# Optimization experiments

Measured on AMD Instinct MI355X. Metric: run time of the kernel, lower is better.

The kernel has to match this reference:

```python
import math
import jax, jax.numpy as jnp
import numpy as np

N_HEADS = 16
TOPK_FACTOR = 0.5

def setup_inputs() -> dict:
    key = jax.random.key(0)
    ks = jax.random.split(key, 11)
    B, L, D = 2, 2048, 1024
    s = 0.02
    return {
        "q": jax.random.normal(ks[0], (B, L, D), jnp.float32),
        "k": jax.random.normal(ks[1], (B, L, D), jnp.float32),
        "v": jax.random.normal(ks[2], (B, L, D), jnp.float32),
        "Wq": jax.random.normal(ks[3], (D, D), jnp.float32) * s,
        "bq": jnp.zeros((D,), jnp.float32),
        "Wk": jax.random.normal(ks[4], (D, D), jnp.float32) * s,
        "bk": jnp.zeros((D,), jnp.float32),
        "Wv": jax.random.normal(ks[5], (D, D), jnp.float32) * s,
        "bv": jnp.zeros((D,), jnp.float32),
        "Wo": jax.random.normal(ks[6], (D, D), jnp.float32) * s,
        "bo": jnp.zeros((D,), jnp.float32),
    }

def reference(q, k, v, Wq, bq, Wk, bk, Wv, bv, Wo, bo):
    B, Lq, D = q.shape
    Lk = k.shape[1]
    H = N_HEADS
    d_k = D // H
    # projections -> [B, H, L, d_k]
    Q = (q @ Wq.T + bq).reshape(B, Lq, H, d_k).transpose(0, 2, 1, 3)
    K = (k @ Wk.T + bk).reshape(B, Lk, H, d_k).transpose(0, 2, 1, 3)
    V = (v @ Wv.T + bv).reshape(B, Lk, H, d_k).transpose(0, 2, 1, 3)
    # dense scores [B, H, Lq, Lk]
    scores = jnp.einsum("bhqd,bhkd->bhqk", Q, K) / math.sqrt(d_k)
    topk = max(1, int(TOPK_FACTOR * Lk))
    topk_scores, topk_idx = jax.lax.top_k(scores, topk)  # [B,H,Lq,topk]
    sm = jax.nn.softmax(topk_scores, axis=-1)
    # scatter softmax probs back into a zero [B,H,Lq,Lk] tensor (dropout in eval = identity)
    b_idx = jnp.arange(B)[:, None, None, None]
    h_idx = jnp.arange(H)[None, :, None, None]
    q_idx = jnp.arange(Lq)[None, None, :, None]
    attn = jnp.zeros_like(scores).at[b_idx, h_idx, q_idx, topk_idx].set(sm)
    ctx = jnp.einsum("bhqk,bhkd->bhqd", attn, V)
    ctx = ctx.transpose(0, 2, 1, 3).reshape(B, Lq, H * d_k)
    return ctx @ Wo.T + bo
```

## Files before the change

kernel.cpp:

```cpp
#include <hip/hip_runtime.h>
#include <math.h>

#define BATCH 2
#define SEQ 2048
#define DM 1024
#define NH 16
#define DH 64
#define TOPKN 1024
#define MROWS (BATCH * SEQ)

typedef float f32x4 __attribute__((ext_vector_type(4)));
typedef short s16x8 __attribute__((ext_vector_type(8)));
typedef short s16x4 __attribute__((ext_vector_type(4)));

#if __has_builtin(__builtin_amdgcn_mfma_f32_16x16x16_bf16)
#define MFMA1616(acc, a, b) acc = __builtin_amdgcn_mfma_f32_16x16x16_bf16(a, b, acc, 0, 0, 0)
#define MFMA1616_FENCE()
#elif __has_builtin(__builtin_amdgcn_mfma_f32_16x16x16bf16_1k)
#define MFMA1616(acc, a, b) acc = __builtin_amdgcn_mfma_f32_16x16x16bf16_1k(a, b, acc, 0, 0, 0)
#define MFMA1616_FENCE()
#else
#define MFMA1616(acc, a, b) \
  asm volatile("v_mfma_f32_16x16x16_bf16 %0, %1, %2, %0" : "+v"(acc) : "v"(a), "v"(b))
#define MFMA1616_FENCE() asm volatile("s_nop 7\ns_nop 7")
#endif

__device__ __forceinline__ unsigned short f2bf(float x) {
  unsigned u = __float_as_uint(x);
  return (unsigned short)((u + 0x7FFFu + ((u >> 16) & 1u)) >> 16);
}
__device__ __forceinline__ unsigned packHL(float x) {
  unsigned h = f2bf(x);
  float r = x - __uint_as_float(h << 16);
  unsigned l = f2bf(r);
  return h | (l << 16);
}

__global__ __launch_bounds__(256) void convW(const float* __restrict__ W,
                                             unsigned short* __restrict__ Whi,
                                             unsigned short* __restrict__ Wlo) {
  int i = (blockIdx.x * 256 + threadIdx.x) * 4;
  float4 x = *(const float4*)&W[i];
  float xs[4] = {x.x, x.y, x.z, x.w};
  union { s16x4 v; unsigned short s[4]; } hu, lu;
#pragma unroll
  for (int e = 0; e < 4; ++e) {
    unsigned short hb = f2bf(xs[e]);
    hu.s[e] = hb;
    lu.s[e] = f2bf(xs[e] - __uint_as_float((unsigned)hb << 16));
  }
  *(s16x4*)&Whi[i] = hu.v;
  *(s16x4*)&Wlo[i] = lu.v;
}

template <int ASRC, int MODE>
__global__ __launch_bounds__(256) void gemm_mfma(
    const void* __restrict__ Asrc, const unsigned short* __restrict__ Whi,
    const unsigned short* __restrict__ Wlo, const float* __restrict__ bias,
    void* __restrict__ out0, void* __restrict__ out1) {
  __shared__ unsigned short Ah[128][64], Al[128][64];
  __shared__ unsigned short Bh[64][64], Bl[64][64];

  const int f = blockIdx.x;
  const int xcd = f & 7, s = f >> 3;
  const int bm = xcd * 4 + (s >> 4);
  const int bn = s & 15;
  const int m0g = bm * 128, n0g = bn * 64;
  const int t = threadIdx.x, w = t >> 6, lane = t & 63;
  const int g = lane >> 4, c = lane & 15;
  const int wm = w >> 1, wn = w & 1;

  f32x4 acc[4][2];
#pragma unroll
  for (int i = 0; i < 4; ++i)
#pragma unroll
    for (int j = 0; j < 2; ++j) acc[i][j] = (f32x4){0.f, 0.f, 0.f, 0.f};

#pragma unroll 1
  for (int k0 = 0; k0 < 1024; k0 += 64) {
#pragma unroll
    for (int i = 0; i < 4; ++i) {
      int oid = t * 4 + i;
      int r = oid >> 3, j = oid & 7;
      union { s16x8 v; unsigned short sh[8]; } hu, lu;
      if (ASRC == 0) {
        const float* src = (const float*)Asrc + (size_t)(m0g + r) * 1024 + k0 + j * 8;
        float4 x0 = *(const float4*)src, x1 = *(const float4*)(src + 4);
        float xs[8] = {x0.x, x0.y, x0.z, x0.w, x1.x, x1.y, x1.z, x1.w};
#pragma unroll
        for (int e = 0; e < 8; ++e) {
          unsigned u = __float_as_uint(xs[e]);
          hu.sh[e] = (unsigned short)(u >> 16);
          lu.sh[e] = f2bf(xs[e] - __uint_as_float(u & 0xFFFF0000u));
        }
      } else {
        const unsigned* src = (const unsigned*)Asrc + (size_t)(m0g + r) * 1024 + k0 + j * 8;
        uint4 u0 = *(const uint4*)src, u1 = *(const uint4*)(src + 4);
        unsigned us[8] = {u0.x, u0.y, u0.z, u0.w, u1.x, u1.y, u1.z, u1.w};
#pragma unroll
        for (int e = 0; e < 8; ++e) {
          hu.sh[e] = (unsigned short)(us[e] & 0xFFFFu);
          lu.sh[e] = (unsigned short)(us[e] >> 16);
        }
      }
      int od = (j ^ (r & 7)) * 8;
      *(s16x8*)&Ah[r][od] = hu.v;
      *(s16x8*)&Al[r][od] = lu.v;
    }
#pragma unroll
    for (int i = 0; i < 4; ++i) {
      int oid = t * 4 + i;
      int pl = oid >> 9, idx = oid & 511, r = idx >> 3, j = idx & 7;
      const unsigned short* src = (pl ? Wlo : Whi) + (size_t)(n0g + r) * 1024 + k0 + j * 8;
      uint4 d = *(const uint4*)src;
      int od = (j ^ (r & 7)) * 8;
      if (pl) *(uint4*)&Bl[r][od] = d; else *(uint4*)&Bh[r][od] = d;
    }
    __syncthreads();
#pragma unroll
    for (int k2 = 0; k2 < 2; ++k2) {
      s16x8 ah[4], al4[4], bh[2], bl[2];
      int ob = ((k2 * 4 + g) ^ (c & 7)) * 8;
#pragma unroll
      for (int i = 0; i < 4; ++i) {
        int r = wm * 64 + i * 16 + c;
        ah[i] = *(const s16x8*)&Ah[r][ob];
        al4[i] = *(const s16x8*)&Al[r][ob];
      }
#pragma unroll
      for (int j = 0; j < 2; ++j) {
        int r = wn * 32 + j * 16 + c;
        bh[j] = *(const s16x8*)&Bh[r][ob];
        bl[j] = *(const s16x8*)&Bl[r][ob];
      }
#pragma unroll
      for (int i = 0; i < 4; ++i)
#pragma unroll
        for (int j = 0; j < 2; ++j) {
          acc[i][j] = __builtin_amdgcn_mfma_f32_16x16x32_bf16(ah[i], bh[j], acc[i][j], 0, 0, 0);
          acc[i][j] = __builtin_amdgcn_mfma_f32_16x16x32_bf16(ah[i], bl[j], acc[i][j], 0, 0, 0);
          acc[i][j] = __builtin_amdgcn_mfma_f32_16x16x32_bf16(al4[i], bh[j], acc[i][j], 0, 0, 0);
        }
    }
    __syncthreads();
  }

#pragma unroll
  for (int j = 0; j < 2; ++j) {
    const int col = n0g + wn * 32 + j * 16 + c;
    const float bj = bias[col];
#pragma unroll
    for (int i = 0; i < 4; ++i) {
      const int row0 = m0g + wm * 64 + i * 16 + g * 4;
      if (MODE == 0) {
        float* O = (float*)out0;
#pragma unroll
        for (int rr = 0; rr < 4; ++rr)
          O[(size_t)(row0 + rr) * 1024 + col] = acc[i][j][rr] + bj;
      } else if (MODE == 1) {
        unsigned* Q = (unsigned*)out0;
#pragma unroll
        for (int rr = 0; rr < 4; ++rr)
          Q[(size_t)(row0 + rr) * 1024 + col] = packHL((acc[i][j][rr] + bj) * 0.125f);
      } else if (MODE == 2) {
        unsigned short* Khi = (unsigned short*)out0;
        unsigned short* Klo = (unsigned short*)out1;
#pragma unroll
        for (int rr = 0; rr < 4; ++rr) {
          float x = acc[i][j][rr] + bj;
          unsigned short hb = f2bf(x);
          Khi[(size_t)(row0 + rr) * 1024 + col] = hb;
          Klo[(size_t)(row0 + rr) * 1024 + col] = f2bf(x - __uint_as_float((unsigned)hb << 16));
        }
      } else {
        unsigned short* Vt = (unsigned short*)out0;
        int b = row0 >> 11, l0 = row0 & (SEQ - 1);
        int h = col >> 6, dh = col & 63;
        union { s16x4 v; unsigned short sh[4]; } vv;
#pragma unroll
        for (int rr = 0; rr < 4; ++rr) vv.sh[rr] = f2bf(acc[i][j][rr] + bj);
        *(s16x4*)&Vt[(((size_t)b * NH + h) * DH + dh) * SEQ + l0] = vv.v;
      }
    }
  }
}

__global__ __launch_bounds__(1024, 4) void attn_mfma(
    const unsigned* __restrict__ QHL, const unsigned short* __restrict__ Khi,
    const unsigned short* __restrict__ Klo, const unsigned short* __restrict__ Vt,
    unsigned* __restrict__ CtxP) {
  __shared__ __align__(16) char smem[16 * 32 * 66 * 4];
  __shared__ __align__(16) float szum[32][16];
  __shared__ unsigned Tlds[32];
  unsigned (*sc)[1028] = (unsigned(*)[1028])smem;
  float (*ctxp)[32][66] = (float(*)[32][66])smem;

  int wg = blockIdx.x;
  wg = (wg & 7) * 256 + (wg >> 3);
  const int bh = wg >> 6, qt = wg & 63;
  const int b = bh >> 4, h = bh & 15;
  const int q0 = qt * 32;
  const int t = threadIdx.x, wid = t >> 6, lane = t & 63;
  const int g = lane >> 4, c = lane & 15;
  const size_t rowb = (size_t)b * SEQ;

  s16x8 qhiA[2], qloA[2], qhiB[2], qloB[2];
#pragma unroll
  for (int qh = 0; qh < 2; ++qh) {
    const unsigned* qp = QHL + (rowb + q0 + qh * 16 + c) * DM + h * DH + g * 8;
#pragma unroll
    for (int ds = 0; ds < 2; ++ds) {
      unsigned uw[8];
      *(uint4*)&uw[0] = *(const uint4*)(qp + ds * 32);
      *(uint4*)&uw[4] = *(const uint4*)(qp + ds * 32 + 4);
      union { s16x8 v; unsigned u[4]; } hi_, lo_;
#pragma unroll
      for (int p = 0; p < 4; ++p) {
        hi_.u[p] = (uw[2 * p] & 0xFFFFu) | (uw[2 * p + 1] << 16);
        lo_.u[p] = (uw[2 * p] >> 16) | (uw[2 * p + 1] & 0xFFFF0000u);
      }
      if (qh == 0) { qhiA[ds] = hi_.v; qloA[ds] = lo_.v; }
      else         { qhiB[ds] = hi_.v; qloB[ds] = lo_.v; }
    }
  }

  unsigned pkA[8][2], pkB[8][2];
  {
    const f32x4 ZZ = (f32x4){0.f, 0.f, 0.f, 0.f};
    const size_t kcol = (size_t)h * DH + g * 8;
#pragma unroll
    for (int tt = 0; tt < 8; ++tt) {
      const size_t krow = (rowb + wid * 128 + tt * 16 + c) * DM + kcol;
      s16x8 kh0 = *(const s16x8*)(Khi + krow);
      s16x8 kh1 = *(const s16x8*)(Khi + krow + 32);
      s16x8 kl0 = *(const s16x8*)(Klo + krow);
      s16x8 kl1 = *(const s16x8*)(Klo + krow + 32);
      f32x4 aA = __builtin_amdgcn_mfma_f32_16x16x32_bf16(kh0, qhiA[0], ZZ, 0, 0, 0);
      f32x4 aB = __builtin_amdgcn_mfma_f32_16x16x32_bf16(kh0, qhiB[0], ZZ, 0, 0, 0);
      aA = __builtin_amdgcn_mfma_f32_16x16x32_bf16(kh1, qhiA[1], aA, 0, 0, 0);
      aB = __builtin_amdgcn_mfma_f32_16x16x32_bf16(kh1, qhiB[1], aB, 0, 0, 0);
      aA = __builtin_amdgcn_mfma_f32_16x16x32_bf16(kl0, qhiA[0], aA, 0, 0, 0);
      aB = __builtin_amdgcn_mfma_f32_16x16x32_bf16(kl0, qhiB[0], aB, 0, 0, 0);
      aA = __builtin_amdgcn_mfma_f32_16x16x32_bf16(kl1, qhiA[1], aA, 0, 0, 0);
      aB = __builtin_amdgcn_mfma_f32_16x16x32_bf16(kl1, qhiB[1], aB, 0, 0, 0);
      aA = __builtin_amdgcn_mfma_f32_16x16x32_bf16(kh0, qloA[0], aA, 0, 0, 0);
      aB = __builtin_amdgcn_mfma_f32_16x16x32_bf16(kh0, qloB[0], aB, 0, 0, 0);
      aA = __builtin_amdgcn_mfma_f32_16x16x32_bf16(kh1, qloA[1], aA, 0, 0, 0);
      aB = __builtin_amdgcn_mfma_f32_16x16x32_bf16(kh1, qloB[1], aB, 0, 0, 0);
      unsigned a0 = (unsigned)fminf(fmaf(aA[0], 8192.f, 32768.5f), 65535.f);
      unsigned a1 = (unsigned)fminf(fmaf(aA[1], 8192.f, 32768.5f), 65535.f);
      unsigned a2 = (unsigned)fminf(fmaf(aA[2], 8192.f, 32768.5f), 65535.f);
      unsigned a3 = (unsigned)fminf(fmaf(aA[3], 8192.f, 32768.5f), 65535.f);
      pkA[tt][0] = a0 | (a1 << 16);
      pkA[tt][1] = a2 | (a3 << 16);
      unsigned b0 = (unsigned)fminf(fmaf(aB[0], 8192.f, 32768.5f), 65535.f);
      unsigned b1 = (unsigned)fminf(fmaf(aB[1], 8192.f, 32768.5f), 65535.f);
      unsigned b2 = (unsigned)fminf(fmaf(aB[2], 8192.f, 32768.5f), 65535.f);
      unsigned b3 = (unsigned)fminf(fmaf(aB[3], 8192.f, 32768.5f), 65535.f);
      pkB[tt][0] = b0 | (b1 << 16);
      pkB[tt][1] = b2 | (b3 << 16);
    }
  }

#pragma unroll
  for (int tt = 0; tt < 8; ++tt) {
    int col = wid * 64 + tt * 8 + g * 2;
    *(uint2*)&sc[c][col] = make_uint2(pkA[tt][0], pkA[tt][1]);
    *(uint2*)&sc[c + 16][col] = make_uint2(pkB[tt][0], pkB[tt][1]);
  }
  __syncthreads();

  {
    const int r = 2 * wid + (lane >> 5);
    const int hl = lane & 31;
    uint4 ts[8];
#pragma unroll
    for (int i = 0; i < 8; ++i)
      ts[i] = *(const uint4*)&sc[r][hl * 4 + i * 128];

    unsigned lo = 30720u, hi = 34816u;
#pragma unroll 1
    for (int it = 0; it < 12; ++it) {
      const unsigned mid = (lo + hi) >> 1;
      int cnt = 0;
#pragma unroll
      for (int i = 0; i < 8; ++i) {
        unsigned a0 = ts[i].x, a1 = ts[i].y, a2 = ts[i].z, a3 = ts[i].w;
        cnt += ((a0 & 0xFFFFu) >= mid) ? 1 : 0;
        cnt += ((a0 >> 16) >= mid) ? 1 : 0;
        cnt += ((a1 & 0xFFFFu) >= mid) ? 1 : 0;
        cnt += ((a1 >> 16) >= mid) ? 1 : 0;
        cnt += ((a2 & 0xFFFFu) >= mid) ? 1 : 0;
        cnt += ((a2 >> 16) >= mid) ? 1 : 0;
        cnt += ((a3 & 0xFFFFu) >= mid) ? 1 : 0;
        cnt += ((a3 >> 16) >= mid) ? 1 : 0;
      }
      cnt += __shfl_xor(cnt, 1);
      cnt += __shfl_xor(cnt, 2);
      cnt += __shfl_xor(cnt, 4);
      cnt += __shfl_xor(cnt, 8);
      cnt += __shfl_xor(cnt, 16);
      bool ge = cnt >= TOPKN;
      lo = ge ? mid : lo;
      hi = ge ? hi : mid;
    }
    if ((lane & 31) == 0) Tlds[r] = lo;
  }
  __syncthreads();
  const unsigned TA = Tlds[c];
  const unsigned TB = Tlds[c + 16];

  const float C1 = 1.44269504f / 8192.0f;
  const float C2 = -49152.0f * (1.44269504f / 8192.0f);
  f32x4 opvA[4], opvB[4];
#pragma unroll
  for (int j = 0; j < 4; ++j) {
    opvA[j] = (f32x4){0.f, 0.f, 0.f, 0.f};
    opvB[j] = (f32x4){0.f, 0.f, 0.f, 0.f};
  }
  float zA = 0.f, zB = 0.f;
  {
    const unsigned short* vb0 = Vt + ((size_t)bh * DH + c) * SEQ + wid * 128 + g * 4;
#pragma unroll
    for (int kt = 0; kt < 8; ++kt) {
      unsigned pa0 = pkA[kt][0], pa1 = pkA[kt][1];
      unsigned ua0 = pa0 & 0xFFFFu, ua1 = pa0 >> 16;
      unsigned ua2 = pa1 & 0xFFFFu, ua3 = pa1 >> 16;
      float ea0 = (ua0 >= TA) ? exp2f(fmaf((float)ua0, C1, C2)) : 0.f;
      float ea1 = (ua1 >= TA) ? exp2f(fmaf((float)ua1, C1, C2)) : 0.f;
      float ea2 = (ua2 >= TA) ? exp2f(fmaf((float)ua2, C1, C2)) : 0.f;
      float ea3 = (ua3 >= TA) ? exp2f(fmaf((float)ua3, C1, C2)) : 0.f;
      zA += (ea0 + ea1) + (ea2 + ea3);
      union { s16x4 v; unsigned u[2]; } pbA;
      pbA.u[0] = ((__float_as_uint(ea0) + 0x8000u) >> 16) |
                 ((__float_as_uint(ea1) + 0x8000u) & 0xFFFF0000u);
      pbA.u[1] = ((__float_as_uint(ea2) + 0x8000u) >> 16) |
                 ((__float_as_uint(ea3) + 0x8000u) & 0xFFFF0000u);
      unsigned pb0 = pkB[kt][0], pb1 = pkB[kt][1];
      unsigned ub0 = pb0 & 0xFFFFu, ub1 = pb0 >> 16;
      unsigned ub2 = pb1 & 0xFFFFu, ub3 = pb1 >> 16;
      float eb0 = (ub0 >= TB) ? exp2f(fmaf((float)ub0, C1, C2)) : 0.f;
      float eb1 = (ub1 >= TB) ? exp2f(fmaf((float)ub1, C1, C2)) : 0.f;
      float eb2 = (ub2 >= TB) ? exp2f(fmaf((float)ub2, C1, C2)) : 0.f;
      float eb3 = (ub3 >= TB) ? exp2f(fmaf((float)ub3, C1, C2)) : 0.f;
      zB += (eb0 + eb1) + (eb2 + eb3);
      union { s16x4 v; unsigned u[2]; } pbB;
      pbB.u[0] = ((__float_as_uint(eb0) + 0x8000u) >> 16) |
                 ((__float_as_uint(eb1) + 0x8000u) & 0xFFFF0000u);
      pbB.u[1] = ((__float_as_uint(eb2) + 0x8000u) >> 16) |
                 ((__float_as_uint(eb3) + 0x8000u) & 0xFFFF0000u);
#pragma unroll
      for (int j = 0; j < 4; ++j) {
        s16x4 va = *(const s16x4*)(vb0 + (size_t)j * 16 * SEQ + kt * 16);
        MFMA1616(opvA[j], va, pbA.v);
        MFMA1616(opvB[j], va, pbB.v);
      }
    }
    MFMA1616_FENCE();
  }

  zA += __shfl_xor(zA, 16);
  zA += __shfl_xor(zA, 32);
  zB += __shfl_xor(zB, 16);
  zB += __shfl_xor(zB, 32);
  if (lane < 16) {
    szum[c][wid] = zA;
    szum[c + 16][wid] = zB;
  }
  __syncthreads();
#pragma unroll
  for (int j = 0; j < 4; ++j) {
    *(f32x4*)&ctxp[wid][c][j * 16 + g * 4] = opvA[j];
    *(f32x4*)&ctxp[wid][c + 16][j * 16 + g * 4] = opvB[j];
  }
  __syncthreads();

  if (t < 512) {
    const int q = t >> 4, d4 = t & 15;
    float4 z0 = *(float4*)&szum[q][0];
    float4 z1 = *(float4*)&szum[q][4];
    float4 z2 = *(float4*)&szum[q][8];
    float4 z3 = *(float4*)&szum[q][12];
    float rinv = 1.f / ((z0.x + z0.y + z0.z + z0.w) + (z1.x + z1.y + z1.z + z1.w) +
                        (z2.x + z2.y + z2.z + z2.w) + (z3.x + z3.y + z3.z + z3.w));
    f32x4 ssum = (f32x4){0.f, 0.f, 0.f, 0.f};
#pragma unroll
    for (int w2 = 0; w2 < 16; ++w2)
      ssum += *(const f32x4*)&ctxp[w2][q][d4 * 4];
    unsigned ov[4];
    ov[0] = packHL(ssum[0] * rinv);
    ov[1] = packHL(ssum[1] * rinv);
    ov[2] = packHL(ssum[2] * rinv);
    ov[3] = packHL(ssum[3] * rinv);
    *(uint4*)&CtxP[(rowb + q0 + q) * DM + h * DH + d4 * 4] = *(uint4*)&ov[0];
  }
}

extern "C" void kernel_launch(void* const* d_in, const int* in_sizes, int n_in,
                              void* d_out, int out_size, void* d_ws, size_t ws_size,
                              hipStream_t stream) {
  const float* q  = (const float*)d_in[0];
  const float* k  = (const float*)d_in[1];
  const float* v  = (const float*)d_in[2];
  const float* Wq = (const float*)d_in[3];
  const float* bq = (const float*)d_in[4];
  const float* Wk = (const float*)d_in[5];
  const float* bk = (const float*)d_in[6];
  const float* Wv = (const float*)d_in[7];
  const float* bv = (const float*)d_in[8];
  const float* Wo = (const float*)d_in[9];
  const float* bo = (const float*)d_in[10];
  float* out = (float*)d_out;

  char* ws = (char*)d_ws;
  unsigned* QHL       = (unsigned*)ws;
  unsigned short* Khi = (unsigned short*)(ws + (16u << 20));
  unsigned short* Klo = (unsigned short*)(ws + (24u << 20));
  unsigned short* Vt  = (unsigned short*)(ws + (32u << 20));
  unsigned short* Whi = (unsigned short*)(ws + (40u << 20));
  unsigned short* Wlo = (unsigned short*)(ws + (42u << 20));

  convW<<<1024, 256, 0, stream>>>(Wq, Whi, Wlo);
  gemm_mfma<0, 1><<<512, 256, 0, stream>>>(q, Whi, Wlo, bq, QHL, nullptr);
  convW<<<1024, 256, 0, stream>>>(Wk, Whi, Wlo);
  gemm_mfma<0, 2><<<512, 256, 0, stream>>>(k, Whi, Wlo, bk, Khi, Klo);
  convW<<<1024, 256, 0, stream>>>(Wv, Whi, Wlo);
  gemm_mfma<0, 3><<<512, 256, 0, stream>>>(v, Whi, Wlo, bv, Vt, nullptr);
  attn_mfma<<<BATCH * NH * (SEQ / 32), 1024, 0, stream>>>(QHL, Khi, Klo, Vt, QHL);
  convW<<<1024, 256, 0, stream>>>(Wo, Whi, Wlo);
  gemm_mfma<1, 0><<<512, 256, 0, stream>>>(QHL, Whi, Wlo, bo, out, nullptr);
}
```

Baseline: 653.1 us.

## Enlarge GEMM tiles, fold score quantization into Q scale, pack-op top-k counting

The projection GEMMs now use 512-thread blocks computing 128x128 tiles instead of 128x64, which halves A-tile reloads and the number of blocks. The A-side hi/lo split uses byte-permute and packed bf16 conversion instructions. In attention, Q is prescaled by 1024 (0.125*8192) and the MFMA accumulator starts at the 32768.5 offset, so score quantization collapses to packed u16 conversions. The threshold-search count uses packed 16-bit saturating subtract and min instead of per-element compares. Risks: the u16 pack saturates rather than clamping with fminf, and the larger blocks give only 256 blocks, which may lower occupancy.

```diff
diff --git a/kernel.cpp b/kernel.cpp
--- a/kernel.cpp
+++ b/kernel.cpp
@@ -12,6 +12,7 @@
 typedef float f32x4 __attribute__((ext_vector_type(4)));
 typedef short s16x8 __attribute__((ext_vector_type(8)));
 typedef short s16x4 __attribute__((ext_vector_type(4)));
+typedef unsigned short u16x2 __attribute__((ext_vector_type(2)));
 
 #if __has_builtin(__builtin_amdgcn_mfma_f32_16x16x16_bf16)
 #define MFMA1616(acc, a, b) acc = __builtin_amdgcn_mfma_f32_16x16x16_bf16(a, b, acc, 0, 0, 0)
@@ -35,6 +36,21 @@
   unsigned l = f2bf(r);
   return h | (l << 16);
 }
+__device__ __forceinline__ unsigned hipair(float a, float b) {
+  return __builtin_amdgcn_perm(__float_as_uint(b), __float_as_uint(a), 0x07060302u);
+}
+__device__ __forceinline__ unsigned lopair(float a, float b) {
+  float ra = a - __uint_as_float(__float_as_uint(a) & 0xFFFF0000u);
+  float rb = b - __uint_as_float(__float_as_uint(b) & 0xFFFF0000u);
+  unsigned out;
+  asm("v_cvt_pk_bf16_f32 %0, %1, %2" : "=v"(out) : "v"(ra), "v"(rb));
+  return out;
+}
+__device__ __forceinline__ unsigned pk_u16(unsigned a, unsigned b) {
+  unsigned out;
+  asm("v_cvt_pk_u16_u32 %0, %1, %2" : "=v"(out) : "v"(a), "v"(b));
+  return out;
+}
 
 __global__ __launch_bounds__(256) void convW(const float* __restrict__ W,
                                              unsigned short* __restrict__ Whi,
@@ -54,21 +70,21 @@
 }
 
 template <int ASRC, int MODE>
-__global__ __launch_bounds__(256) void gemm_mfma(
+__global__ __launch_bounds__(512) void gemm_mfma(
     const void* __restrict__ Asrc, const unsigned short* __restrict__ Whi,
     const unsigned short* __restrict__ Wlo, const float* __restrict__ bias,
     void* __restrict__ out0, void* __restrict__ out1) {
   __shared__ unsigned short Ah[128][64], Al[128][64];
-  __shared__ unsigned short Bh[64][64], Bl[64][64];
+  __shared__ unsigned short Bh[128][64], Bl[128][64];
 
   const int f = blockIdx.x;
-  const int xcd = f & 7, s = f >> 3;
-  const int bm = xcd * 4 + (s >> 4);
-  const int bn = s & 15;
-  const int m0g = bm * 128, n0g = bn * 64;
+  const int xcd = f & 7, r_ = f >> 3;
+  const int bm = xcd * 4 + (r_ >> 3);
+  const int bn = r_ & 7;
+  const int m0g = bm * 128, n0g = bn * 128;
   const int t = threadIdx.x, w = t >> 6, lane = t & 63;
   const int g = lane >> 4, c = lane & 15;
-  const int wm = w >> 1, wn = w & 1;
+  const int wm = w >> 2, wn = w & 3;
 
   f32x4 acc[4][2];
 #pragma unroll
@@ -79,42 +95,41 @@
 #pragma unroll 1
   for (int k0 = 0; k0 < 1024; k0 += 64) {
 #pragma unroll
+    for (int i = 0; i < 2; ++i) {
+      int oid = t * 2 + i;
+      int rr = oid >> 3, j = oid & 7;
+      unsigned hw[4], lw[4];
+      if (ASRC == 0) {
+        const float* src = (const float*)Asrc + (size_t)(m0g + rr) * 1024 + k0 + j * 8;
+        float4 x0 = *(const float4*)src, x1 = *(const float4*)(src + 4);
+        float xs[8] = {x0.x, x0.y, x0.z, x0.w, x1.x, x1.y, x1.z, x1.w};
+#pragma unroll
+        for (int p = 0; p < 4; ++p) {
+          hw[p] = hipair(xs[2 * p], xs[2 * p + 1]);
+          lw[p] = lopair(xs[2 * p], xs[2 * p + 1]);
+        }
+      } else {
+        const unsigned* src = (const unsigned*)Asrc + (size_t)(m0g + rr) * 1024 + k0 + j * 8;
+        uint4 u0 = *(const uint4*)src, u1 = *(const uint4*)(src + 4);
+        unsigned us[8] = {u0.x, u0.y, u0.z, u0.w, u1.x, u1.y, u1.z, u1.w};
+#pragma unroll
+        for (int p = 0; p < 4; ++p) {
+          hw[p] = __builtin_amdgcn_perm(us[2 * p + 1], us[2 * p], 0x05040100u);
+          lw[p] = __builtin_amdgcn_perm(us[2 * p + 1], us[2 * p], 0x07060302u);
+        }
+      }
+      int od = (j ^ (rr & 7)) * 8;
+      *(uint4*)&Ah[rr][od] = make_uint4(hw[0], hw[1], hw[2], hw[3]);
+      *(uint4*)&Al[rr][od] = make_uint4(lw[0], lw[1], lw[2], lw[3]);
+    }
+#pragma unroll
     for (int i = 0; i < 4; ++i) {
       int oid = t * 4 + i;
-      int r = oid >> 3, j = oid & 7;
-      union { s16x8 v; unsigned short sh[8]; } hu, lu;
-      if (ASRC == 0) {
-        const float* src = (const float*)Asrc + (size_t)(m0g + r) * 1024 + k0 + j * 8;
-        float4 x0 = *(const float4*)src, x1 = *(const float4*)(src + 4);
-        float xs[8] = {x0.x, x0.y, x0.z, x0.w, x1.x, x1.y, x1.z, x1.w};
-#pragma unroll
-        for (int e = 0; e < 8; ++e) {
-          unsigned u = __float_as_uint(xs[e]);
-          hu.sh[e] = (unsigned short)(u >> 16);
-          lu.sh[e] = f2bf(xs[e] - __uint_as_float(u & 0xFFFF0000u));
-        }
-      } else {
-        const unsigned* src = (const unsigned*)Asrc + (size_t)(m0g + r) * 1024 + k0 + j * 8;
-        uint4 u0 = *(const uint4*)src, u1 = *(const uint4*)(src + 4);
-        unsigned us[8] = {u0.x, u0.y, u0.z, u0.w, u1.x, u1.y, u1.z, u1.w};
-#pragma unroll
-        for (int e = 0; e < 8; ++e) {
-          hu.sh[e] = (unsigned short)(us[e] & 0xFFFFu);
-          lu.sh[e] = (unsigned short)(us[e] >> 16);
-        }
-      }
-      int od = (j ^ (r & 7)) * 8;
-      *(s16x8*)&Ah[r][od] = hu.v;
-      *(s16x8*)&Al[r][od] = lu.v;
-    }
-#pragma unroll
-    for (int i = 0; i < 4; ++i) {
-      int oid = t * 4 + i;
-      int pl = oid >> 9, idx = oid & 511, r = idx >> 3, j = idx & 7;
-      const unsigned short* src = (pl ? Wlo : Whi) + (size_t)(n0g + r) * 1024 + k0 + j * 8;
+      int pl = oid >> 10, idx = oid & 1023, rr = idx >> 3, j = idx & 7;
+      const unsigned short* src = (pl ? Wlo : Whi) + (size_t)(n0g + rr) * 1024 + k0 + j * 8;
       uint4 d = *(const uint4*)src;
-      int od = (j ^ (r & 7)) * 8;
-      if (pl) *(uint4*)&Bl[r][od] = d; else *(uint4*)&Bh[r][od] = d;
+      int od = (j ^ (rr & 7)) * 8;
+      if (pl) *(uint4*)&Bl[rr][od] = d; else *(uint4*)&Bh[rr][od] = d;
     }
     __syncthreads();
 #pragma unroll
@@ -123,15 +138,15 @@
       int ob = ((k2 * 4 + g) ^ (c & 7)) * 8;
 #pragma unroll
       for (int i = 0; i < 4; ++i) {
-        int r = wm * 64 + i * 16 + c;
-        ah[i] = *(const s16x8*)&Ah[r][ob];
-        al4[i] = *(const s16x8*)&Al[r][ob];
+        int rr = wm * 64 + i * 16 + c;
+        ah[i] = *(const s16x8*)&Ah[rr][ob];
+        al4[i] = *(const s16x8*)&Al[rr][ob];
       }
 #pragma unroll
       for (int j = 0; j < 2; ++j) {
-        int r = wn * 32 + j * 16 + c;
-        bh[j] = *(const s16x8*)&Bh[r][ob];
-        bl[j] = *(const s16x8*)&Bl[r][ob];
+        int rr = wn * 32 + j * 16 + c;
+        bh[j] = *(const s16x8*)&Bh[rr][ob];
+        bl[j] = *(const s16x8*)&Bl[rr][ob];
       }
 #pragma unroll
       for (int i = 0; i < 4; ++i)
@@ -161,7 +176,7 @@
         unsigned* Q = (unsigned*)out0;
 #pragma unroll
         for (int rr = 0; rr < 4; ++rr)
-          Q[(size_t)(row0 + rr) * 1024 + col] = packHL((acc[i][j][rr] + bj) * 0.125f);
+          Q[(size_t)(row0 + rr) * 1024 + col] = packHL((acc[i][j][rr] + bj) * 1024.0f);
       } else if (MODE == 2) {
         unsigned short* Khi = (unsigned short*)out0;
         unsigned short* Klo = (unsigned short*)out1;
@@ -226,7 +241,7 @@
 
   unsigned pkA[8][2], pkB[8][2];
   {
-    const f32x4 ZZ = (f32x4){0.f, 0.f, 0.f, 0.f};
+    const f32x4 INIT = (f32x4){32768.5f, 32768.5f, 32768.5f, 32768.5f};
     const size_t kcol = (size_t)h * DH + g * 8;
 #pragma unroll
     for (int tt = 0; tt < 8; ++tt) {
@@ -235,8 +250,8 @@
       s16x8 kh1 = *(const s16x8*)(Khi + krow + 32);
       s16x8 kl0 = *(const s16x8*)(Klo + krow);
       s16x8 kl1 = *(const s16x8*)(Klo + krow + 32);
-      f32x4 aA = __builtin_amdgcn_mfma_f32_16x16x32_bf16(kh0, qhiA[0], ZZ, 0, 0, 0);
-      f32x4 aB = __builtin_amdgcn_mfma_f32_16x16x32_bf16(kh0, qhiB[0], ZZ, 0, 0, 0);
+      f32x4 aA = __builtin_amdgcn_mfma_f32_16x16x32_bf16(kh0, qhiA[0], INIT, 0, 0, 0);
+      f32x4 aB = __builtin_amdgcn_mfma_f32_16x16x32_bf16(kh0, qhiB[0], INIT, 0, 0, 0);
       aA = __builtin_amdgcn_mfma_f32_16x16x32_bf16(kh1, qhiA[1], aA, 0, 0, 0);
       aB = __builtin_amdgcn_mfma_f32_16x16x32_bf16(kh1, qhiB[1], aB, 0, 0, 0);
       aA = __builtin_amdgcn_mfma_f32_16x16x32_bf16(kl0, qhiA[0], aA, 0, 0, 0);
@@ -247,18 +262,10 @@
       aB = __builtin_amdgcn_mfma_f32_16x16x32_bf16(kh0, qloB[0], aB, 0, 0, 0);
       aA = __builtin_amdgcn_mfma_f32_16x16x32_bf16(kh1, qloA[1], aA, 0, 0, 0);
       aB = __builtin_amdgcn_mfma_f32_16x16x32_bf16(kh1, qloB[1], aB, 0, 0, 0);
-      unsigned a0 = (unsigned)fminf(fmaf(aA[0], 8192.f, 32768.5f), 65535.f);
-      unsigned a1 = (unsigned)fminf(fmaf(aA[1], 8192.f, 32768.5f), 65535.f);
-      unsigned a2 = (unsigned)fminf(fmaf(aA[2], 8192.f, 32768.5f), 65535.f);
-      unsigned a3 = (unsigned)fminf(fmaf(aA[3], 8192.f, 32768.5f), 65535.f);
-      pkA[tt][0] = a0 | (a1 << 16);
-      pkA[tt][1] = a2 | (a3 << 16);
-      unsigned b0 = (unsigned)fminf(fmaf(aB[0], 8192.f, 32768.5f), 65535.f);
-      unsigned b1 = (unsigned)fminf(fmaf(aB[1], 8192.f, 32768.5f), 65535.f);
-      unsigned b2 = (unsigned)fminf(fmaf(aB[2], 8192.f, 32768.5f), 65535.f);
-      unsigned b3 = (unsigned)fminf(fmaf(aB[3], 8192.f, 32768.5f), 65535.f);
-      pkB[tt][0] = b0 | (b1 << 16);
-      pkB[tt][1] = b2 | (b3 << 16);
+      pkA[tt][0] = pk_u16((unsigned)aA[0], (unsigned)aA[1]);
+      pkA[tt][1] = pk_u16((unsigned)aA[2], (unsigned)aA[3]);
+      pkB[tt][0] = pk_u16((unsigned)aB[0], (unsigned)aB[1]);
+      pkB[tt][1] = pk_u16((unsigned)aB[2], (unsigned)aB[3]);
     }
   }
 
@@ -282,19 +289,22 @@
 #pragma unroll 1
     for (int it = 0; it < 12; ++it) {
       const unsigned mid = (lo + hi) >> 1;
-      int cnt = 0;
+      const unsigned short mm = (unsigned short)(mid - 1u);
+      u16x2 m2 = {mm, mm};
+      const u16x2 one2 = {1, 1};
+      u16x2 a2 = {0, 0};
 #pragma unroll
       for (int i = 0; i < 8; ++i) {
-        unsigned a0 = ts[i].x, a1 = ts[i].y, a2 = ts[i].z, a3 = ts[i].w;
-        cnt += ((a0 & 0xFFFFu) >= mid) ? 1 : 0;
-        cnt += ((a0 >> 16) >= mid) ? 1 : 0;
-        cnt += ((a1 & 0xFFFFu) >= mid) ? 1 : 0;
-        cnt += ((a1 >> 16) >= mid) ? 1 : 0;
-        cnt += ((a2 & 0xFFFFu) >= mid) ? 1 : 0;
-        cnt += ((a2 >> 16) >= mid) ? 1 : 0;
-        cnt += ((a3 & 0xFFFFu) >= mid) ? 1 : 0;
-        cnt += ((a3 >> 16) >= mid) ? 1 : 0;
-      }
+        a2 += __builtin_elementwise_min(
+            __builtin_elementwise_sub_sat(__builtin_bit_cast(u16x2, ts[i].x), m2), one2);
+        a2 += __builtin_elementwise_min(
+            __builtin_elementwise_sub_sat(__builtin_bit_cast(u16x2, ts[i].y), m2), one2);
+        a2 += __builtin_elementwise_min(
+            __builtin_elementwise_sub_sat(__builtin_bit_cast(u16x2, ts[i].z), m2), one2);
+        a2 += __builtin_elementwise_min(
+            __builtin_elementwise_sub_sat(__builtin_bit_cast(u16x2, ts[i].w), m2), one2);
+      }
+      int cnt = (int)a2.x + (int)a2.y;
       cnt += __shfl_xor(cnt, 1);
       cnt += __shfl_xor(cnt, 2);
       cnt += __shfl_xor(cnt, 4);
@@ -421,12 +431,12 @@
   unsigned short* Wlo = (unsigned short*)(ws + (42u << 20));
 
   convW<<<1024, 256, 0, stream>>>(Wq, Whi, Wlo);
-  gemm_mfma<0, 1><<<512, 256, 0, stream>>>(q, Whi, Wlo, bq, QHL, nullptr);
+  gemm_mfma<0, 1><<<256, 512, 0, stream>>>(q, Whi, Wlo, bq, QHL, nullptr);
   convW<<<1024, 256, 0, stream>>>(Wk, Whi, Wlo);
-  gemm_mfma<0, 2><<<512, 256, 0, stream>>>(k, Whi, Wlo, bk, Khi, Klo);
+  gemm_mfma<0, 2><<<256, 512, 0, stream>>>(k, Whi, Wlo, bk, Khi, Klo);
   convW<<<1024, 256, 0, stream>>>(Wv, Whi, Wlo);
-  gemm_mfma<0, 3><<<512, 256, 0, stream>>>(v, Whi, Wlo, bv, Vt, nullptr);
+  gemm_mfma<0, 3><<<256, 512, 0, stream>>>(v, Whi, Wlo, bv, Vt, nullptr);
   attn_mfma<<<BATCH * NH * (SEQ / 32), 1024, 0, stream>>>(QHL, Khi, Klo, Vt, QHL);
   convW<<<1024, 256, 0, stream>>>(Wo, Whi, Wlo);
-  gemm_mfma<1, 0><<<512, 256, 0, stream>>>(QHL, Whi, Wlo, bo, out, nullptr);
-}
+  gemm_mfma<1, 0><<<256, 512, 0, stream>>>(QHL, Whi, Wlo, bo, out, nullptr);
+}
```

Result: no change. 642.5 us (-1.6%).
